# Performance work log

Hardware: AMD Instinct MI355X
Metric: run time of the kernel (lower is better)

## Reference

```python
import jax, jax.numpy as jnp
import numpy as np

DIM_HIDDEN = 512
NUM_CLASSES = 100
LAMBDA_C = 1.0
POOL = 8  # Maha_distance pools the feature dim into 8 groups


def setup_inputs() -> dict:
    key = jax.random.key(0)
    k1, k2, k3 = jax.random.split(key, 3)
    B = 1024
    hidden = jax.random.normal(k1, (B, DIM_HIDDEN), dtype=jnp.float32)
    feature_center = jax.random.normal(k2, (NUM_CLASSES, DIM_HIDDEN), dtype=jnp.float32)
    y = jax.random.randint(k3, (B,), 0, NUM_CLASSES, dtype=jnp.int64 if jax.config.jax_enable_x64 else jnp.int32)
    return {"hidden": hidden, "feature_center": feature_center, "y": y}


def _batch_cov(points):
    # points: [B, N, D] -> [B, D, D]; matches torch batch_cov (sum of outer products / (N-1))
    B, N, D = points.shape
    diffs = points - points.mean(axis=1, keepdims=True)
    return jnp.einsum('bnd,bne->bde', diffs, diffs) / (N - 1)


def _maha_distance(X, Y):
    # X, Y: [bs, a, b]
    bs, a, b = X.shape
    X = X.reshape(bs, a, POOL, b // POOL).mean(axis=3)  # [bs, a, 8]
    Y = Y.reshape(bs, a, POOL, b // POOL).mean(axis=3)
    X = X / (jnp.linalg.norm(X, axis=2, keepdims=True) + 1e-6)
    Y = Y / (jnp.linalg.norm(Y, axis=2, keepdims=True) + 1e-6)
    XY = jnp.concatenate([X, Y], axis=1)  # [bs, 2a, 8]
    bcov = _batch_cov(XY)                 # [bs, 8, 8]
    pinv_cov = jnp.linalg.pinv(bcov, hermitian=True)
    X_Y = X - Y                           # [bs, a, 8]
    m_dis = jnp.einsum('bad,bde,bae->ba', X_Y, pinv_cov, X_Y)
    return jnp.sqrt(m_dis)


def reference(hidden, feature_center, y):
    B = hidden.shape[0]
    one_y = jax.nn.one_hot(y, NUM_CLASSES, dtype=hidden.dtype)
    center = jnp.broadcast_to(feature_center[None, :, :], (B, NUM_CLASSES, DIM_HIDDEN))
    c_feature = jnp.broadcast_to(hidden[:, None, :], (B, NUM_CLASSES, DIM_HIDDEN))
    dis = _maha_distance(c_feature, center)  # [B, C]
    intra_maha = jnp.sum(dis * one_y, axis=1)
    inter_maha = jnp.sum(dis * (1.0 - one_y), axis=1) / (NUM_CLASSES - 1)
    loss = intra_maha + LAMBDA_C * (-inter_maha)
    return loss.mean()
```

## Files before the change

kernel.cpp:

```cpp
#include <hip/hip_runtime.h>
#include <math.h>


#define DIMH 512
#define NC   100
#define PG   8
#define GS   64
#define RPB  4

__global__ __launch_bounds__(256) void ccl_main_kernel(
    const float* __restrict__ hidden,
    const float* __restrict__ fc,
    const int*   __restrict__ y,
    double* __restrict__ partials,
    int B)
{
    __shared__ float  cn[NC][PG];
    __shared__ float  cbarS[PG];
    __shared__ float  SinvS[64];
    __shared__ double Am[8][16];
    __shared__ double wpart[RPB];

    const int tid  = threadIdx.x;
    const int lane = tid & 63;
    const int wave = tid >> 6;
    const int b    = blockIdx.x * RPB + wave;

    float4 h0 = make_float4(0.f, 0.f, 0.f, 0.f);
    float4 h1 = make_float4(0.f, 0.f, 0.f, 0.f);
    int yt = -1;
    if (b < B) {
        const float4* hrow = reinterpret_cast<const float4*>(hidden + (size_t)b * DIMH) + lane * 2;
        h0 = hrow[0];
        h1 = hrow[1];
        yt = y[b];
    }

    for (int c = wave; c < NC; c += RPB) {
        const float4* row = reinterpret_cast<const float4*>(fc + (size_t)c * DIMH) + lane * 2;
        float4 a = row[0];
        float4 d = row[1];
        float s = a.x + a.y + a.z + a.w + d.x + d.y + d.z + d.w;
        s += __shfl_xor(s, 1);
        s += __shfl_xor(s, 2);
        s += __shfl_xor(s, 4);
        if ((lane & 7) == 0) cn[c][lane >> 3] = s * (1.0f / GS);
    }
    __syncthreads();

    if (tid < NC) {
        float v[PG];
        float n2 = 0.0f;
#pragma unroll
        for (int g = 0; g < PG; ++g) { v[g] = cn[tid][g]; n2 += v[g] * v[g]; }
        float inv = 1.0f / (sqrtf(n2) + 1e-6f);
#pragma unroll
        for (int g = 0; g < PG; ++g) cn[tid][g] = v[g] * inv;
    }
    __syncthreads();

    if (tid < PG) {
        float s = 0.0f;
        for (int c = 0; c < NC; ++c) s += cn[c][tid];
        cbarS[tid] = s * (1.0f / NC);
    }
    __syncthreads();

    const int i = tid >> 3, j = tid & 7;
    if (tid < 64) {
        float ci = cbarS[i], cj = cbarS[j];
        double s = 0.0;
        for (int c = 0; c < NC; ++c)
            s += (double)(cn[c][i] - ci) * (double)(cn[c][j] - cj);
        Am[i][j]     = s;
        Am[i][j + 8] = (i == j) ? 1.0 : 0.0;
    }
    __syncthreads();

#pragma unroll 1
    for (int k = 0; k < 8; ++k) {
        double piv = (tid < 64) ? Am[k][k] : 1.0;
        __syncthreads();
        if (tid < 64 && i == k) { Am[k][j] /= piv; Am[k][j + 8] /= piv; }
        __syncthreads();
        double f    = (tid < 64) ? Am[i][k]     : 0.0;
        double akj  = (tid < 64) ? Am[k][j]     : 0.0;
        double akj8 = (tid < 64) ? Am[k][j + 8] : 0.0;
        __syncthreads();
        if (tid < 64 && i != k) { Am[i][j] -= f * akj; Am[i][j + 8] -= f * akj8; }
        __syncthreads();
    }
    if (tid < 64) SinvS[tid] = (float)Am[i][j + 8];
    __syncthreads();

    double loss_b = 0.0;
    if (b < B) {
        float s = h0.x + h0.y + h0.z + h0.w + h1.x + h1.y + h1.z + h1.w;
        s += __shfl_xor(s, 1);
        s += __shfl_xor(s, 2);
        s += __shfl_xor(s, 4);

        float hn[PG];
        float n2 = 0.0f;
#pragma unroll
        for (int g = 0; g < PG; ++g) {
            hn[g] = __shfl(s, g << 3) * (1.0f / GS);
            n2 += hn[g] * hn[g];
        }
        float inv = 1.0f / (sqrtf(n2) + 1e-6f);
#pragma unroll
        for (int g = 0; g < PG; ++g) hn[g] *= inv;

        float u[PG], w[PG];
#pragma unroll
        for (int g = 0; g < PG; ++g) u[g] = hn[g] - cbarS[g];
        float uw = 0.0f;
#pragma unroll
        for (int ii = 0; ii < PG; ++ii) {
            float t = 0.0f;
#pragma unroll
            for (int jj = 0; jj < PG; ++jj) t += SinvS[ii * 8 + jj] * u[jj];
            w[ii] = t;
            uw += u[ii] * t;
        }
        const float coef = 50.0f / (1.0f + 50.0f * uw);

        float sumd = 0.0f, disy = 0.0f;
        for (int c = lane; c < NC; c += 64) {
            float v[PG];
#pragma unroll
            for (int g = 0; g < PG; ++g) v[g] = hn[g] - cn[c][g];
            float q1 = 0.0f, q2 = 0.0f;
#pragma unroll
            for (int ii = 0; ii < PG; ++ii) {
                float t = 0.0f;
#pragma unroll
                for (int jj = 0; jj < PG; ++jj) t += SinvS[ii * 8 + jj] * v[jj];
                q1 += v[ii] * t;
                q2 += v[ii] * w[ii];
            }
            float m = 199.0f * (q1 - coef * q2 * q2);
            float d = sqrtf(fmaxf(m, 0.0f));
            sumd += d;
            if (c == yt) disy = d;
        }
#pragma unroll
        for (int off = 1; off < 64; off <<= 1) {
            sumd += __shfl_xor(sumd, off);
            disy += __shfl_xor(disy, off);
        }
        loss_b = (double)disy - (double)(sumd - disy) * (1.0 / 99.0);
    }

    if (lane == 0) wpart[wave] = loss_b;
    __syncthreads();

    if (tid == 0)
        partials[blockIdx.x] = wpart[0] + wpart[1] + wpart[2] + wpart[3];
}

__global__ __launch_bounds__(256) void ccl_finalize_kernel(
    const double* __restrict__ partials, float* __restrict__ out, int n, int B)
{
    __shared__ double sh[4];
    const int tid = threadIdx.x, lane = tid & 63, wave = tid >> 6;
    double v = (tid < n) ? partials[tid] : 0.0;
#pragma unroll
    for (int off = 1; off < 64; off <<= 1) v += __shfl_xor(v, off);
    if (lane == 0) sh[wave] = v;
    __syncthreads();
    if (tid == 0) out[0] = (float)((sh[0] + sh[1] + sh[2] + sh[3]) / (double)B);
}

extern "C" void kernel_launch(void* const* d_in, const int* in_sizes, int n_in,
                              void* d_out, int out_size, void* d_ws, size_t ws_size,
                              hipStream_t stream)
{
    const float* hidden = (const float*)d_in[0];
    const float* fc     = (const float*)d_in[1];
    const int*   y      = (const int*)d_in[2];
    float*       out    = (float*)d_out;

    const int B = in_sizes[0] / DIMH;
    const int nblocks = (B + RPB - 1) / RPB;

    double* partials = (double*)d_ws;

    ccl_main_kernel<<<nblocks, 256, 0, stream>>>(hidden, fc, y, partials, B);
    ccl_finalize_kernel<<<1, 256, 0, stream>>>(partials, out, nblocks, B);
}
```

Before: 76.88 us.

## Invert class scatter matrix in registers with wave shuffles instead of LDS

The per-block 8x8 Gauss-Jordan inversion now runs in fp32 registers inside a single wave and exchanges values with shuffles. This replaces the fp64 shared-memory version, which needed four block barriers per pivot step. The scatter matrix is computed as raw second moments split across all four waves, then corrected with the mean outer product, and the class mean is reduced in parallel by one wave. This removes about 32 barriers and the fp64 arithmetic from every block. In exchange the uncentered fp32 formulation carries a cancellation and precision risk.

```diff
diff --git a/kernel.cpp b/kernel.cpp
--- a/kernel.cpp
+++ b/kernel.cpp
@@ -18,7 +18,7 @@
     __shared__ float  cn[NC][PG];
     __shared__ float  cbarS[PG];
     __shared__ float  SinvS[64];
-    __shared__ double Am[8][16];
+    __shared__ float  Spart[RPB][64];
     __shared__ double wpart[RPB];
 
     const int tid  = threadIdx.x;
@@ -59,38 +59,41 @@
     }
     __syncthreads();
 
-    if (tid < PG) {
+    if (wave == 1) {
+        const int g = lane & 7, t = lane >> 3;
         float s = 0.0f;
-        for (int c = 0; c < NC; ++c) s += cn[c][tid];
-        cbarS[tid] = s * (1.0f / NC);
+        for (int c = t; c < NC; c += 8) s += cn[c][g];
+        s += __shfl_xor(s, 8);
+        s += __shfl_xor(s, 16);
+        s += __shfl_xor(s, 32);
+        if (t == 0) cbarS[g] = s * (1.0f / NC);
+    }
+    {
+        const int i = lane >> 3, j = lane & 7;
+        const int c0 = wave * (NC / RPB);
+        float s = 0.0f;
+        for (int c = c0; c < c0 + NC / RPB; ++c) s += cn[c][i] * cn[c][j];
+        Spart[wave][lane] = s;
     }
     __syncthreads();
 
-    const int i = tid >> 3, j = tid & 7;
-    if (tid < 64) {
-        float ci = cbarS[i], cj = cbarS[j];
-        double s = 0.0;
-        for (int c = 0; c < NC; ++c)
-            s += (double)(cn[c][i] - ci) * (double)(cn[c][j] - cj);
-        Am[i][j]     = s;
-        Am[i][j + 8] = (i == j) ? 1.0 : 0.0;
+    if (wave == 0) {
+        const int i = lane >> 3, j = lane & 7;
+        float a = Spart[0][lane] + Spart[1][lane] + Spart[2][lane] + Spart[3][lane]
+                - (float)NC * cbarS[i] * cbarS[j];
+        float binv = (i == j) ? 1.0f : 0.0f;
+#pragma unroll
+        for (int k = 0; k < 8; ++k) {
+            float akk = __shfl(a,    k * 8 + k);
+            float aik = __shfl(a,    i * 8 + k);
+            float akj = __shfl(a,    k * 8 + j);
+            float bkj = __shfl(binv, k * 8 + j);
+            float r = 1.0f / akk;
+            if (i == k) { a *= r;            binv *= r; }
+            else        { float f = aik * r; a -= f * akj; binv -= f * bkj; }
+        }
+        SinvS[lane] = binv;
     }
-    __syncthreads();
-
-#pragma unroll 1
-    for (int k = 0; k < 8; ++k) {
-        double piv = (tid < 64) ? Am[k][k] : 1.0;
-        __syncthreads();
-        if (tid < 64 && i == k) { Am[k][j] /= piv; Am[k][j + 8] /= piv; }
-        __syncthreads();
-        double f    = (tid < 64) ? Am[i][k]     : 0.0;
-        double akj  = (tid < 64) ? Am[k][j]     : 0.0;
-        double akj8 = (tid < 64) ? Am[k][j + 8] : 0.0;
-        __syncthreads();
-        if (tid < 64 && i != k) { Am[i][j] -= f * akj; Am[i][j + 8] -= f * akj8; }
-        __syncthreads();
-    }
-    if (tid < 64) SinvS[tid] = (float)Am[i][j + 8];
     __syncthreads();
 
     double loss_b = 0.0;
```

Result: faster. 70.54 us (-8.2%).
